# Performance work log

Hardware: AMD Instinct MI355X
Metric: run time of the kernel (lower is better)

## Reference

```python
import jax, jax.numpy as jnp
import numpy as np

B, N_BLOCK, D_MODEL = 4096, 64, 256


def setup_inputs() -> dict:
    key = jax.random.key(0)
    k1, k2 = jax.random.split(key)
    h = jax.random.normal(k1, (B, N_BLOCK, D_MODEL), dtype=jnp.float32)
    # xavier_normal_ for square [d, d]: std = sqrt(2/(d+d)) = 1/sqrt(d)
    W_a = jax.random.normal(k2, (D_MODEL, D_MODEL), dtype=jnp.float32) / jnp.sqrt(
        jnp.float32(D_MODEL))
    b_a = jnp.zeros((N_BLOCK, D_MODEL), dtype=jnp.float32)
    return {"h": h, "W_a": W_a, "b_a": b_a}


def reference(h, W_a, b_a):
    # h: [B, n_block, d_model]
    # scores = tanh(h @ W_a + b_a): [B, n_block, d_model]
    s = jnp.tanh(jnp.einsum("bnd,de->bne", h, W_a) + b_a)
    # Original applies Softmax(dim=1) to a [1, n_block, d_model] chunk,
    # i.e. normalization is over the n_block axis.
    a = jax.nn.softmax(s, axis=1)
    # elementwise weight then full sum per block -> [B, n_block]
    return jnp.sum(a * h, axis=2)
```

## Files before the change

### kernel.cpp

```cpp
#include <hip/hip_runtime.h>
#include <hip/hip_bf16.h>

#define BATCH 4096
#define NB    64
#define DM    256
#define KSW   8
#define KST   10

typedef __bf16 bf16x8 __attribute__((ext_vector_type(8)));
typedef float  f32x4  __attribute__((ext_vector_type(4)));

union Frag16 { uint4 u; bf16x8 b; ushort s[8]; };
union Pk2    { __hip_bfloat162 v; unsigned u; };

__device__ __forceinline__ ushort f2bf(float x) {
    unsigned u = __float_as_uint(x);
    return (ushort)((u + 0x7FFFu + ((u >> 16) & 1u)) >> 16);
}
__device__ __forceinline__ unsigned pk2(float a, float b) {
    Pk2 p; p.v = __float22bfloat162_rn(make_float2(a, b));
    return p.u;
}
__device__ __forceinline__ float bf2f(ushort u) {
    return __uint_as_float(((unsigned)u) << 16);
}

__global__ void swizzle_WB(const float* __restrict__ W, const float* __restrict__ ba,
                           ushort* __restrict__ Wf) {
    int idx  = blockIdx.x * 256 + threadIdx.x;
    int lane = idx & 63;
    int g    = idx >> 6;
    int et   = g / KST;
    int ks   = g % KST;
    int e    = et * 16 + (lane & 15);
    int r0   = (ks < KSW) ? ks * 32 : (ks - KSW) * 32;
    r0 += ((lane >> 4) << 3);
    const float* src = (ks < KSW) ? W : ba;
    Frag16 f;
#pragma unroll
    for (int j = 0; j < 8; ++j)
        f.s[j] = f2bf(src[(r0 + j) * DM + e]);
    reinterpret_cast<uint4*>(Wf)[idx] = f.u;
}

__global__ __launch_bounds__(256, 4) void aspect_attn(
    const float*  __restrict__ h,
    const ushort* __restrict__ Wf,
    float*        __restrict__ out)
{
    __shared__ __align__(16) ushort Hs[2048 * 8];
    __shared__ float op[4][NB];

    const int tid  = threadIdx.x;
    const int wave = tid >> 6;
    const int lane = tid & 63;
    const int quad = lane >> 4;
    const int l15  = lane & 15;
    const int b    = blockIdx.x;

    const float* hb = h + (size_t)b * (NB * DM);

#pragma unroll
    for (int it = 0; it < 8; ++it) {
        int slot = it * 256 + tid;
        int f    = slot >> 6;
        int row  = ((f >> 3) << 4) | l15;
        int k0   = ((f & 7) << 5) | (quad << 3);
        const f32x4* p = reinterpret_cast<const f32x4*>(hb + row * DM + k0);
        f32x4 a = p[0], c = p[1];
        uint4 o;
        o.x = pk2(a.x, a.y); o.y = pk2(a.z, a.w);
        o.z = pk2(c.x, c.y); o.w = pk2(c.z, c.w);
        reinterpret_cast<uint4*>(Hs)[slot] = o;
    }
    __syncthreads();

    f32x4 acc[4][4];
#pragma unroll
    for (int mt = 0; mt < 4; ++mt)
#pragma unroll
        for (int nt = 0; nt < 4; ++nt) {
            f32x4 z = {0.f, 0.f, 0.f, 0.f};
            acc[mt][nt] = z;
        }

    const uint4* WfB = reinterpret_cast<const uint4*>(Wf);
    const uint4* HsB = reinterpret_cast<const uint4*>(Hs);

#pragma unroll
    for (int ks = 0; ks < KSW; ++ks) {
        Frag16 af[4], bfr[4];
#pragma unroll
        for (int mt = 0; mt < 4; ++mt)
            af[mt].u = HsB[(mt * 8 + ks) * 64 + lane];
#pragma unroll
        for (int nt = 0; nt < 4; ++nt)
            bfr[nt].u = WfB[((wave * 4 + nt) * KST + ks) * 64 + lane];
#pragma unroll
        for (int mt = 0; mt < 4; ++mt)
#pragma unroll
            for (int nt = 0; nt < 4; ++nt)
                acc[mt][nt] = __builtin_amdgcn_mfma_f32_16x16x32_bf16(
                    af[mt].b, bfr[nt].b, acc[mt][nt], 0, 0, 0);
    }
#pragma unroll
    for (int kx = 0; kx < 2; ++kx) {
        Frag16 af[4], bfr[4];
#pragma unroll
        for (int nt = 0; nt < 4; ++nt)
            bfr[nt].u = WfB[((wave * 4 + nt) * KST + KSW + kx) * 64 + lane];
        const int kb = kx * 32 + quad * 8;
#pragma unroll
        for (int mt = 0; mt < 4; ++mt) {
            int d = (mt * 16 + l15) - kb;
#pragma unroll
            for (int j = 0; j < 8; ++j)
                af[mt].s[j] = (d == j) ? (ushort)0x3F80 : (ushort)0;
        }
#pragma unroll
        for (int mt = 0; mt < 4; ++mt)
#pragma unroll
            for (int nt = 0; nt < 4; ++nt)
                acc[mt][nt] = __builtin_amdgcn_mfma_f32_16x16x32_bf16(
                    af[mt].b, bfr[nt].b, acc[mt][nt], 0, 0, 0);
    }

#pragma unroll
    for (int mt = 0; mt < 4; ++mt)
#pragma unroll
        for (int nt = 0; nt < 4; ++nt)
#pragma unroll
            for (int r = 0; r < 4; ++r) {
                float x = acc[mt][nt][r];
                float e = __expf(-2.f * fabsf(x));
                float t = (1.f - e) * __builtin_amdgcn_rcpf(1.f + e);
                acc[mt][nt][r] = copysignf(t, x);
            }

#pragma unroll
    for (int nt = 0; nt < 4; ++nt) {
        float ls = 0.f;
#pragma unroll
        for (int mt = 0; mt < 4; ++mt)
#pragma unroll
            for (int r = 0; r < 4; ++r) {
                float p = __expf(acc[mt][nt][r]);
                acc[mt][nt][r] = p;
                ls += p;
            }
        ls += __shfl_xor(ls, 16, 64);
        ls += __shfl_xor(ls, 32, 64);
        float inv = __builtin_amdgcn_rcpf(ls);
#pragma unroll
        for (int mt = 0; mt < 4; ++mt)
#pragma unroll
            for (int r = 0; r < 4; ++r)
                acc[mt][nt][r] *= inv;
    }

    const int colb = wave * 64;
#pragma unroll
    for (int mt = 0; mt < 4; ++mt)
#pragma unroll
        for (int r = 0; r < 4; ++r) {
            const int row  = mt * 16 + quad * 4 + r;
            const int ridx = mt * 4096 + (quad * 4 + r) * 8;
            float s = 0.f;
#pragma unroll
            for (int nt = 0; nt < 4; ++nt) {
                int col  = colb + nt * 16 + l15;
                int coff = (col >> 5) * 512 + ((col >> 3) & 3) * 128 + (col & 7);
                s += acc[mt][nt][r] * bf2f(Hs[ridx + coff]);
            }
#pragma unroll
            for (int m = 1; m < 16; m <<= 1)
                s += __shfl_xor(s, m, 64);
            if (l15 == 0) op[wave][row] = s;
        }
    __syncthreads();

    if (tid < NB)
        out[(size_t)b * NB + tid] = op[0][tid] + op[1][tid] + op[2][tid] + op[3][tid];
}

extern "C" void kernel_launch(void* const* d_in, const int* in_sizes, int n_in,
                              void* d_out, int out_size, void* d_ws, size_t ws_size,
                              hipStream_t stream) {
    const float* h  = (const float*)d_in[0];
    const float* W  = (const float*)d_in[1];
    const float* ba = (const float*)d_in[2];
    float* out = (float*)d_out;
    ushort* Wf = (ushort*)d_ws;

    swizzle_WB<<<40, 256, 0, stream>>>(W, ba, Wf);
    aspect_attn<<<BATCH, 256, 0, stream>>>(h, Wf, out);
}
```

Baseline: 406.8 us.

## Process eight batches per block with double-buffered register prefetch of h

Each workgroup now handles eight batch items in a loop. The global loads for the next item are issued into registers before the current item's MFMA work, then converted and written into a second shared-memory buffer, which hides load latency. The cross-wave shared reduction is replaced by atomicAdd into an output that is zeroed by a memset. This adds a memset launch and many atomics, raises register pressure (launch bounds 2), and cuts the grid to 512 blocks.

New measurement: 521.4 us. 1.28x slower.

```diff
diff --git a/kernel.cpp b/kernel.cpp
--- a/kernel.cpp
+++ b/kernel.cpp
@@ -6,6 +6,8 @@
 #define DM    256
 #define KSW   8
 #define KST   10
+#define NBPB  8
+#define GRID  (BATCH / NBPB)
 
 typedef __bf16 bf16x8 __attribute__((ext_vector_type(8)));
 typedef float  f32x4  __attribute__((ext_vector_type(4)));
@@ -43,144 +45,178 @@
     reinterpret_cast<uint4*>(Wf)[idx] = f.u;
 }
 
-__global__ __launch_bounds__(256, 4) void aspect_attn(
+__global__ __launch_bounds__(256, 2) void aspect_attn(
     const float*  __restrict__ h,
     const ushort* __restrict__ Wf,
     float*        __restrict__ out)
 {
-    __shared__ __align__(16) ushort Hs[2048 * 8];
-    __shared__ float op[4][NB];
+    __shared__ __align__(16) ushort Hs[2 * 16384];
 
     const int tid  = threadIdx.x;
     const int wave = tid >> 6;
     const int lane = tid & 63;
     const int quad = lane >> 4;
     const int l15  = lane & 15;
-    const int b    = blockIdx.x;
-
-    const float* hb = h + (size_t)b * (NB * DM);
-
+    const int b0   = blockIdx.x * NBPB;
+
+    const uint4* WfB = reinterpret_cast<const uint4*>(Wf);
+
+    int goff[8];
 #pragma unroll
     for (int it = 0; it < 8; ++it) {
-        int slot = it * 256 + tid;
-        int f    = slot >> 6;
-        int row  = ((f >> 3) << 4) | l15;
-        int k0   = ((f & 7) << 5) | (quad << 3);
-        const f32x4* p = reinterpret_cast<const f32x4*>(hb + row * DM + k0);
-        f32x4 a = p[0], c = p[1];
-        uint4 o;
-        o.x = pk2(a.x, a.y); o.y = pk2(a.z, a.w);
-        o.z = pk2(c.x, c.y); o.w = pk2(c.z, c.w);
-        reinterpret_cast<uint4*>(Hs)[slot] = o;
+        int f = it * 4 + wave;
+        int row = ((f >> 3) << 4) | l15;
+        int k0  = ((f & 7) << 5) | (quad << 3);
+        goff[it] = row * DM + k0;
+    }
+
+    {
+        const float* hb = h + (size_t)b0 * (NB * DM);
+#pragma unroll
+        for (int it = 0; it < 8; ++it) {
+            const f32x4* p = reinterpret_cast<const f32x4*>(hb + goff[it]);
+            f32x4 a = p[0], c = p[1];
+            uint4 o;
+            o.x = pk2(a.x, a.y); o.y = pk2(a.z, a.w);
+            o.z = pk2(c.x, c.y); o.w = pk2(c.z, c.w);
+            reinterpret_cast<uint4*>(Hs)[it * 256 + tid] = o;
+        }
     }
     __syncthreads();
 
-    f32x4 acc[4][4];
-#pragma unroll
-    for (int mt = 0; mt < 4; ++mt)
+    int cur = 0;
+    for (int i = 0; i < NBPB; ++i) {
+        const int b = b0 + i;
+
+        f32x4 ld[16];
+        const bool havenext = (i + 1 < NBPB);
+        if (havenext) {
+            const float* hn = h + (size_t)(b + 1) * (NB * DM);
+#pragma unroll
+            for (int it = 0; it < 8; ++it) {
+                const f32x4* p = reinterpret_cast<const f32x4*>(hn + goff[it]);
+                ld[2 * it]     = p[0];
+                ld[2 * it + 1] = p[1];
+            }
+        }
+
+        f32x4 acc[4][4];
+#pragma unroll
+        for (int mt = 0; mt < 4; ++mt)
+#pragma unroll
+            for (int nt = 0; nt < 4; ++nt) {
+                f32x4 z = {0.f, 0.f, 0.f, 0.f};
+                acc[mt][nt] = z;
+            }
+
+        const uint4* HsB = reinterpret_cast<const uint4*>(Hs) + cur * 2048;
+#pragma unroll
+        for (int ks = 0; ks < KSW; ++ks) {
+            Frag16 af[4], bfr[4];
+#pragma unroll
+            for (int mt = 0; mt < 4; ++mt)
+                af[mt].u = HsB[(mt * 8 + ks) * 64 + lane];
+#pragma unroll
+            for (int nt = 0; nt < 4; ++nt)
+                bfr[nt].u = WfB[((wave * 4 + nt) * KST + ks) * 64 + lane];
+#pragma unroll
+            for (int mt = 0; mt < 4; ++mt)
+#pragma unroll
+                for (int nt = 0; nt < 4; ++nt)
+                    acc[mt][nt] = __builtin_amdgcn_mfma_f32_16x16x32_bf16(
+                        af[mt].b, bfr[nt].b, acc[mt][nt], 0, 0, 0);
+        }
+#pragma unroll
+        for (int kx = 0; kx < 2; ++kx) {
+            Frag16 af[4], bfr[4];
+#pragma unroll
+            for (int nt = 0; nt < 4; ++nt)
+                bfr[nt].u = WfB[((wave * 4 + nt) * KST + KSW + kx) * 64 + lane];
+            const int kb = kx * 32 + quad * 8;
+#pragma unroll
+            for (int mt = 0; mt < 4; ++mt) {
+                int d = (mt * 16 + l15) - kb;
+#pragma unroll
+                for (int j = 0; j < 8; ++j)
+                    af[mt].s[j] = (d == j) ? (ushort)0x3F80 : (ushort)0;
+            }
+#pragma unroll
+            for (int mt = 0; mt < 4; ++mt)
+#pragma unroll
+                for (int nt = 0; nt < 4; ++nt)
+                    acc[mt][nt] = __builtin_amdgcn_mfma_f32_16x16x32_bf16(
+                        af[mt].b, bfr[nt].b, acc[mt][nt], 0, 0, 0);
+        }
+
+#pragma unroll
+        for (int mt = 0; mt < 4; ++mt)
+#pragma unroll
+            for (int nt = 0; nt < 4; ++nt)
+#pragma unroll
+                for (int r = 0; r < 4; ++r) {
+                    float x = acc[mt][nt][r];
+                    float e = __expf(-2.f * fabsf(x));
+                    float t = (1.f - e) * __builtin_amdgcn_rcpf(1.f + e);
+                    acc[mt][nt][r] = copysignf(t, x);
+                }
+
 #pragma unroll
         for (int nt = 0; nt < 4; ++nt) {
-            f32x4 z = {0.f, 0.f, 0.f, 0.f};
-            acc[mt][nt] = z;
-        }
-
-    const uint4* WfB = reinterpret_cast<const uint4*>(Wf);
-    const uint4* HsB = reinterpret_cast<const uint4*>(Hs);
-
-#pragma unroll
-    for (int ks = 0; ks < KSW; ++ks) {
-        Frag16 af[4], bfr[4];
+            float ls = 0.f;
+#pragma unroll
+            for (int mt = 0; mt < 4; ++mt)
+#pragma unroll
+                for (int r = 0; r < 4; ++r) {
+                    float p = __expf(acc[mt][nt][r]);
+                    acc[mt][nt][r] = p;
+                    ls += p;
+                }
+            ls += __shfl_xor(ls, 16, 64);
+            ls += __shfl_xor(ls, 32, 64);
+            float inv = __builtin_amdgcn_rcpf(ls);
+#pragma unroll
+            for (int mt = 0; mt < 4; ++mt)
+#pragma unroll
+                for (int r = 0; r < 4; ++r)
+                    acc[mt][nt][r] *= inv;
+        }
+
+        const int colb = wave * 64;
+        const ushort* Hcur = Hs + cur * 16384;
 #pragma unroll
         for (int mt = 0; mt < 4; ++mt)
-            af[mt].u = HsB[(mt * 8 + ks) * 64 + lane];
-#pragma unroll
-        for (int nt = 0; nt < 4; ++nt)
-            bfr[nt].u = WfB[((wave * 4 + nt) * KST + ks) * 64 + lane];
-#pragma unroll
-        for (int mt = 0; mt < 4; ++mt)
-#pragma unroll
-            for (int nt = 0; nt < 4; ++nt)
-                acc[mt][nt] = __builtin_amdgcn_mfma_f32_16x16x32_bf16(
-                    af[mt].b, bfr[nt].b, acc[mt][nt], 0, 0, 0);
+#pragma unroll
+            for (int r = 0; r < 4; ++r) {
+                const int row  = mt * 16 + quad * 4 + r;
+                const int ridx = mt * 4096 + (quad * 4 + r) * 8;
+                float s = 0.f;
+#pragma unroll
+                for (int nt = 0; nt < 4; ++nt) {
+                    int col  = colb + nt * 16 + l15;
+                    int coff = (col >> 5) * 512 + ((col >> 3) & 3) * 128 + (col & 7);
+                    s += acc[mt][nt][r] * bf2f(Hcur[ridx + coff]);
+                }
+#pragma unroll
+                for (int m = 1; m < 16; m <<= 1)
+                    s += __shfl_xor(s, m, 64);
+                if (l15 == 0)
+                    atomicAdd(out + (size_t)b * NB + row, s);
+            }
+
+        if (havenext) {
+            uint4* dst = reinterpret_cast<uint4*>(Hs) + (cur ^ 1) * 2048;
+#pragma unroll
+            for (int it = 0; it < 8; ++it) {
+                f32x4 a = ld[2 * it], c = ld[2 * it + 1];
+                uint4 o;
+                o.x = pk2(a.x, a.y); o.y = pk2(a.z, a.w);
+                o.z = pk2(c.x, c.y); o.w = pk2(c.z, c.w);
+                dst[it * 256 + tid] = o;
+            }
+        }
+        __syncthreads();
+        cur ^= 1;
     }
-#pragma unroll
-    for (int kx = 0; kx < 2; ++kx) {
-        Frag16 af[4], bfr[4];
-#pragma unroll
-        for (int nt = 0; nt < 4; ++nt)
-            bfr[nt].u = WfB[((wave * 4 + nt) * KST + KSW + kx) * 64 + lane];
-        const int kb = kx * 32 + quad * 8;
-#pragma unroll
-        for (int mt = 0; mt < 4; ++mt) {
-            int d = (mt * 16 + l15) - kb;
-#pragma unroll
-            for (int j = 0; j < 8; ++j)
-                af[mt].s[j] = (d == j) ? (ushort)0x3F80 : (ushort)0;
-        }
-#pragma unroll
-        for (int mt = 0; mt < 4; ++mt)
-#pragma unroll
-            for (int nt = 0; nt < 4; ++nt)
-                acc[mt][nt] = __builtin_amdgcn_mfma_f32_16x16x32_bf16(
-                    af[mt].b, bfr[nt].b, acc[mt][nt], 0, 0, 0);
-    }
-
-#pragma unroll
-    for (int mt = 0; mt < 4; ++mt)
-#pragma unroll
-        for (int nt = 0; nt < 4; ++nt)
-#pragma unroll
-            for (int r = 0; r < 4; ++r) {
-                float x = acc[mt][nt][r];
-                float e = __expf(-2.f * fabsf(x));
-                float t = (1.f - e) * __builtin_amdgcn_rcpf(1.f + e);
-                acc[mt][nt][r] = copysignf(t, x);
-            }
-
-#pragma unroll
-    for (int nt = 0; nt < 4; ++nt) {
-        float ls = 0.f;
-#pragma unroll
-        for (int mt = 0; mt < 4; ++mt)
-#pragma unroll
-            for (int r = 0; r < 4; ++r) {
-                float p = __expf(acc[mt][nt][r]);
-                acc[mt][nt][r] = p;
-                ls += p;
-            }
-        ls += __shfl_xor(ls, 16, 64);
-        ls += __shfl_xor(ls, 32, 64);
-        float inv = __builtin_amdgcn_rcpf(ls);
-#pragma unroll
-        for (int mt = 0; mt < 4; ++mt)
-#pragma unroll
-            for (int r = 0; r < 4; ++r)
-                acc[mt][nt][r] *= inv;
-    }
-
-    const int colb = wave * 64;
-#pragma unroll
-    for (int mt = 0; mt < 4; ++mt)
-#pragma unroll
-        for (int r = 0; r < 4; ++r) {
-            const int row  = mt * 16 + quad * 4 + r;
-            const int ridx = mt * 4096 + (quad * 4 + r) * 8;
-            float s = 0.f;
-#pragma unroll
-            for (int nt = 0; nt < 4; ++nt) {
-                int col  = colb + nt * 16 + l15;
-                int coff = (col >> 5) * 512 + ((col >> 3) & 3) * 128 + (col & 7);
-                s += acc[mt][nt][r] * bf2f(Hs[ridx + coff]);
-            }
-#pragma unroll
-            for (int m = 1; m < 16; m <<= 1)
-                s += __shfl_xor(s, m, 64);
-            if (l15 == 0) op[wave][row] = s;
-        }
-    __syncthreads();
-
-    if (tid < NB)
-        out[(size_t)b * NB + tid] = op[0][tid] + op[1][tid] + op[2][tid] + op[3][tid];
 }
 
 extern "C" void kernel_launch(void* const* d_in, const int* in_sizes, int n_in,
@@ -192,6 +228,7 @@
     float* out = (float*)d_out;
     ushort* Wf = (ushort*)d_ws;
 
+    hipMemsetAsync(out, 0, (size_t)out_size * sizeof(float), stream);
     swizzle_WB<<<40, 256, 0, stream>>>(W, ba, Wf);
-    aspect_attn<<<BATCH, 256, 0, stream>>>(h, Wf, out);
-}
+    aspect_attn<<<GRID, 256, 0, stream>>>(h, Wf, out);
+}
```

## Drop LDS staging of h, load A fragments from global, atomic output reduce

Applied to the files above, without the earlier changes.

Removes the shared-memory staging of the h block: MFMA A fragments are loaded directly from global memory and converted to bf16 per k-step, and the epilogue reads h in fp32 from global again. The cross-wave LDS reduction and its barriers are replaced by atomicAdd into a zeroed output, which adds a memset launch. Tanh is replaced by a rational Padé approximation clamped to ±1 and fused with exp2 for the softmax, and the occupancy hint is lowered from 4 to 3. The intent is to cut LDS traffic, barriers and transcendental cost, at the price of four waves each re-reading h from global/L2 and a looser tanh approximation.

Measured after the change: 473.1 us. +16.3%, slower.

```diff
diff --git a/kernel.cpp b/kernel.cpp
--- a/kernel.cpp
+++ b/kernel.cpp
@@ -21,9 +21,6 @@
     Pk2 p; p.v = __float22bfloat162_rn(make_float2(a, b));
     return p.u;
 }
-__device__ __forceinline__ float bf2f(ushort u) {
-    return __uint_as_float(((unsigned)u) << 16);
-}
 
 __global__ void swizzle_WB(const float* __restrict__ W, const float* __restrict__ ba,
                            ushort* __restrict__ Wf) {
@@ -43,14 +40,11 @@
     reinterpret_cast<uint4*>(Wf)[idx] = f.u;
 }
 
-__global__ __launch_bounds__(256, 4) void aspect_attn(
+__global__ __launch_bounds__(256, 3) void aspect_attn(
     const float*  __restrict__ h,
     const ushort* __restrict__ Wf,
     float*        __restrict__ out)
 {
-    __shared__ __align__(16) ushort Hs[2048 * 8];
-    __shared__ float op[4][NB];
-
     const int tid  = threadIdx.x;
     const int wave = tid >> 6;
     const int lane = tid & 63;
@@ -58,22 +52,13 @@
     const int l15  = lane & 15;
     const int b    = blockIdx.x;
 
-    const float* hb = h + (size_t)b * (NB * DM);
+    const float* hb  = h + (size_t)b * (NB * DM);
+    const uint4* WfB = reinterpret_cast<const uint4*>(Wf);
 
+    int offA[4];
 #pragma unroll
-    for (int it = 0; it < 8; ++it) {
-        int slot = it * 256 + tid;
-        int f    = slot >> 6;
-        int row  = ((f >> 3) << 4) | l15;
-        int k0   = ((f & 7) << 5) | (quad << 3);
-        const f32x4* p = reinterpret_cast<const f32x4*>(hb + row * DM + k0);
-        f32x4 a = p[0], c = p[1];
-        uint4 o;
-        o.x = pk2(a.x, a.y); o.y = pk2(a.z, a.w);
-        o.z = pk2(c.x, c.y); o.w = pk2(c.z, c.w);
-        reinterpret_cast<uint4*>(Hs)[slot] = o;
-    }
-    __syncthreads();
+    for (int mt = 0; mt < 4; ++mt)
+        offA[mt] = (mt * 16 + l15) * DM + quad * 8;
 
     f32x4 acc[4][4];
 #pragma unroll
@@ -84,15 +69,16 @@
             acc[mt][nt] = z;
         }
 
-    const uint4* WfB = reinterpret_cast<const uint4*>(Wf);
-    const uint4* HsB = reinterpret_cast<const uint4*>(Hs);
-
 #pragma unroll
     for (int ks = 0; ks < KSW; ++ks) {
         Frag16 af[4], bfr[4];
 #pragma unroll
-        for (int mt = 0; mt < 4; ++mt)
-            af[mt].u = HsB[(mt * 8 + ks) * 64 + lane];
+        for (int mt = 0; mt < 4; ++mt) {
+            const f32x4* p = reinterpret_cast<const f32x4*>(hb + offA[mt] + ks * 32);
+            f32x4 a = p[0], c = p[1];
+            af[mt].u.x = pk2(a.x, a.y); af[mt].u.y = pk2(a.z, a.w);
+            af[mt].u.z = pk2(c.x, c.y); af[mt].u.w = pk2(c.z, c.w);
+        }
 #pragma unroll
         for (int nt = 0; nt < 4; ++nt)
             bfr[nt].u = WfB[((wave * 4 + nt) * KST + ks) * 64 + lane];
@@ -125,18 +111,7 @@
                     af[mt].b, bfr[nt].b, acc[mt][nt], 0, 0, 0);
     }
 
-#pragma unroll
-    for (int mt = 0; mt < 4; ++mt)
-#pragma unroll
-        for (int nt = 0; nt < 4; ++nt)
-#pragma unroll
-            for (int r = 0; r < 4; ++r) {
-                float x = acc[mt][nt][r];
-                float e = __expf(-2.f * fabsf(x));
-                float t = (1.f - e) * __builtin_amdgcn_rcpf(1.f + e);
-                acc[mt][nt][r] = copysignf(t, x);
-            }
-
+    const float L2E = 1.4426950408889634f;
 #pragma unroll
     for (int nt = 0; nt < 4; ++nt) {
         float ls = 0.f;
@@ -144,7 +119,13 @@
         for (int mt = 0; mt < 4; ++mt)
 #pragma unroll
             for (int r = 0; r < 4; ++r) {
-                float p = __expf(acc[mt][nt][r]);
+                float x  = acc[mt][nt][r];
+                float x2 = x * x;
+                float nu = x * __builtin_fmaf(x2 + 105.f, x2, 945.f);
+                float de = __builtin_fmaf(__builtin_fmaf(x2, 15.f, 420.f), x2, 945.f);
+                float t  = nu * __builtin_amdgcn_rcpf(de) * L2E;
+                t = fminf(fmaxf(t, -L2E), L2E);
+                float p = __builtin_amdgcn_exp2f(t);
                 acc[mt][nt][r] = p;
                 ls += p;
             }
@@ -163,24 +144,19 @@
     for (int mt = 0; mt < 4; ++mt)
 #pragma unroll
         for (int r = 0; r < 4; ++r) {
-            const int row  = mt * 16 + quad * 4 + r;
-            const int ridx = mt * 4096 + (quad * 4 + r) * 8;
+            const int row = mt * 16 + quad * 4 + r;
             float s = 0.f;
 #pragma unroll
             for (int nt = 0; nt < 4; ++nt) {
-                int col  = colb + nt * 16 + l15;
-                int coff = (col >> 5) * 512 + ((col >> 3) & 3) * 128 + (col & 7);
-                s += acc[mt][nt][r] * bf2f(Hs[ridx + coff]);
+                int col = colb + nt * 16 + l15;
+                s += acc[mt][nt][r] * hb[row * DM + col];
             }
 #pragma unroll
             for (int m = 1; m < 16; m <<= 1)
                 s += __shfl_xor(s, m, 64);
-            if (l15 == 0) op[wave][row] = s;
+            if (l15 == 0)
+                atomicAdd(out + (size_t)b * NB + row, s);
         }
-    __syncthreads();
-
-    if (tid < NB)
-        out[(size_t)b * NB + tid] = op[0][tid] + op[1][tid] + op[2][tid] + op[3][tid];
 }
 
 extern "C" void kernel_launch(void* const* d_in, const int* in_sizes, int n_in,
@@ -192,6 +168,7 @@
     float* out = (float*)d_out;
     ushort* Wf = (ushort*)d_ws;
 
+    hipMemsetAsync(out, 0, (size_t)out_size * sizeof(float), stream);
     swizzle_WB<<<40, 256, 0, stream>>>(W, ba, Wf);
     aspect_attn<<<BATCH, 256, 0, stream>>>(h, Wf, out);
 }
```
